# Performance work log

Measured on AMD Instinct MI355X. Metric: run time of the kernel, lower is better.

## Reference

```python
import jax, jax.numpy as jnp
import numpy as np

N_HEAD = 16
N_EMBD = 1024
B, T = 4, 1024


def setup_inputs() -> dict:
    key = jax.random.key(0)
    ks = jax.random.split(key, 8)
    hs = N_EMBD // N_HEAD
    x = jax.random.normal(ks[0], (B, T, N_EMBD), dtype=jnp.float32)
    # previous-layer attention load per token, ~O(1/T) like a softmax column mean
    refractory_state = jax.random.uniform(ks[1], (B, T), dtype=jnp.float32) / T
    s_attn = 1.0 / np.sqrt(N_EMBD)
    W_attn = jax.random.normal(ks[2], (N_EMBD, 3 * N_EMBD), dtype=jnp.float32) * s_attn
    b_attn = jnp.zeros((3 * N_EMBD,), dtype=jnp.float32)
    W_proj = jax.random.normal(ks[3], (N_EMBD, N_EMBD), dtype=jnp.float32) * s_attn
    b_proj = jnp.zeros((N_EMBD,), dtype=jnp.float32)
    # learnable LIF params, init per module (lif_mode='refractory')
    threshold = jnp.full((N_HEAD,), 0.01, dtype=jnp.float32)
    leak = jnp.full((N_HEAD,), 2.0, dtype=jnp.float32)
    steepness = jnp.full((N_HEAD,), 2.0, dtype=jnp.float32)
    ref_strength = jnp.full((N_HEAD,), -2.0, dtype=jnp.float32)
    cross_w = jnp.full((N_HEAD,), -2.0, dtype=jnp.float32)
    return {
        "x": x, "refractory_state": refractory_state,
        "W_attn": W_attn, "b_attn": b_attn,
        "W_proj": W_proj, "b_proj": b_proj,
        "threshold": threshold, "leak": leak, "steepness": steepness,
        "ref_strength": ref_strength, "cross_w": cross_w,
    }


def reference(x, refractory_state, W_attn, b_attn, W_proj, b_proj,
              threshold, leak, steepness, ref_strength, cross_w):
    Bq, Tq, C = x.shape
    H = N_HEAD
    hs = C // H
    qkv = x @ W_attn + b_attn                     # [B,T,3C]
    q, k, v = jnp.split(qkv, 3, axis=-1)
    q = q.reshape(Bq, Tq, H, hs).transpose(0, 2, 1, 3)  # [B,H,T,hs]
    k = k.reshape(Bq, Tq, H, hs).transpose(0, 2, 1, 3)
    v = v.reshape(Bq, Tq, H, hs).transpose(0, 2, 1, 3)

    att = jnp.einsum('bhqd,bhkd->bhqk', q, k) * (1.0 / jnp.sqrt(jnp.asarray(hs, x.dtype)))
    causal = jnp.tril(jnp.ones((Tq, Tq), dtype=bool))
    att = jnp.where(causal[None, None], att, -jnp.inf)
    probs = jax.nn.softmax(att, axis=-1)          # [B,H,T,T]

    thr = (jnp.abs(threshold) * 0.1)[None, :, None, None]
    lk = jax.nn.sigmoid(leak)[None, :, None, None]
    st = jax.nn.softplus(steepness)[None, :, None, None]
    # refractory: column load over queries + cross-layer load
    column_load = probs.mean(axis=-2, keepdims=True)          # [B,H,1,T]
    eff_thr = thr + jax.nn.softplus(ref_strength)[None, :, None, None] * column_load
    eff_thr = eff_thr + jax.nn.sigmoid(cross_w)[None, :, None, None] * refractory_state[:, None, None, :]

    fire = jax.nn.sigmoid(st * (probs - eff_thr))
    lif_w = fire + lk * (1.0 - fire)
    mod = probs * lif_w
    mod = mod / (mod.sum(axis=-1, keepdims=True) + 1e-8)
    new_refractory = mod.mean(axis=1).mean(axis=-2)           # [B,T]

    y = jnp.einsum('bhqk,bhkd->bhqd', mod, v)
    y = y.transpose(0, 2, 1, 3).reshape(Bq, Tq, C)
    y = y @ W_proj + b_proj
    return y, new_refractory
```

## Files before the change

kernel.cpp:

```cpp
#include <hip/hip_runtime.h>
#include <math.h>

#define B_  4
#define T_  1024
#define C_  1024
#define H_  16
#define HS_ 64
#define K2E 0.1803368801f
#define LOG2E 1.44269504f

typedef _Float16 f16;
typedef _Float16 f16x8 __attribute__((ext_vector_type(8)));
typedef _Float16 f16x4 __attribute__((ext_vector_type(4)));
typedef float f32x4 __attribute__((ext_vector_type(4)));

#define MFMA16(a,b,c) __builtin_amdgcn_mfma_f32_16x16x32_f16(a,b,c,0,0,0)
#define EXP2(x) __builtin_amdgcn_exp2f(x)
#define RCP(x)  __builtin_amdgcn_rcpf(x)

#define PSTRIDE_BH 557056

__device__ __forceinline__ float qsum_(float v){
    v += __shfl_xor(v,1,64); v += __shfl_xor(v,2,64);
    v += __shfl_xor(v,4,64); v += __shfl_xor(v,8,64);
    return v;
}
__device__ __forceinline__ float sigmoidf_(float x){ return 1.0f/(1.0f + __expf(-x)); }
__device__ __forceinline__ float softplusf_(float x){ return fmaxf(x, 0.0f) + log1pf(__expf(-fabsf(x))); }

__device__ __forceinline__ void gload_lds16(const f16* g, f16* l){
    __builtin_amdgcn_global_load_lds(
        (__attribute__((address_space(1))) void*)(void*)g,
        (__attribute__((address_space(3))) void*)(void*)l, 16, 0, 0);
}

__global__ __launch_bounds__(256) void prep_k(
    const float* __restrict__ x, const float* __restrict__ Wa,
    const float* __restrict__ Wp,
    f16* __restrict__ x_h, f16* __restrict__ WaT, f16* __restrict__ WpT,
    float* __restrict__ zbase)
{
    __shared__ float tl[32][33];
    const int bid = blockIdx.x, tid = threadIdx.x;
    if (bid < 2048){
        int i = bid*256 + tid;
        const float4* p = (const float4*)x + (size_t)i*2;
        float4 a = p[0], b = p[1];
        f16x8 o;
        o[0]=(f16)a.x; o[1]=(f16)a.y; o[2]=(f16)a.z; o[3]=(f16)a.w;
        o[4]=(f16)b.x; o[5]=(f16)b.y; o[6]=(f16)b.z; o[7]=(f16)b.w;
        *((f16x8*)x_h + i) = o;
    } else if (bid < 5120){
        int t = bid - 2048;
        int n0 = (t % 96)*32, k0 = (t / 96)*32;
        const int c = tid & 31, r4 = tid >> 5;
        #pragma unroll
        for (int i=0;i<4;i++){ int r = r4*4+i; tl[r][c] = Wa[(size_t)(k0+r)*3072 + n0 + c]; }
        __syncthreads();
        #pragma unroll
        for (int i=0;i<4;i++){ int r = r4*4+i; WaT[(size_t)(n0+r)*1024 + k0 + c] = (f16)tl[c][r]; }
    } else if (bid < 6144){
        int t = bid - 5120;
        int n0 = (t & 31)*32, k0 = (t >> 5)*32;
        const int c = tid & 31, r4 = tid >> 5;
        #pragma unroll
        for (int i=0;i<4;i++){ int r = r4*4+i; tl[r][c] = Wp[(size_t)(k0+r)*1024 + n0 + c]; }
        __syncthreads();
        #pragma unroll
        for (int i=0;i<4;i++){ int r = r4*4+i; WpT[(size_t)(n0+r)*1024 + k0 + c] = (f16)tl[c][r]; }
    } else {
        int idx = (bid - 6144)*256 + tid;
        float4 z; z.x=0.f; z.y=0.f; z.z=0.f; z.w=0.f;
        ((float4*)zbase)[idx] = z;
    }
}

#define CT_STRIDE 132
__global__ __launch_bounds__(256) void gemm_qkv_k(
    const f16* __restrict__ A, const f16* __restrict__ Bt,
    const float* __restrict__ bias,
    f16* __restrict__ Qh, f16* __restrict__ Kh, f16* __restrict__ Vt)
{
    __shared__ __align__(16) f16 smem[16896];
    const int tid = threadIdx.x;
    const int lane = tid & 63, wave = tid >> 6;
    const int lx = lane & 15, quad = lane >> 4;
    const int wm = wave & 1, wn = wave >> 1;
    const int lin = blockIdx.y*24 + blockIdx.x;
    const int nb  = (lin & 7)*96 + (lin >> 3);
    const int m0 = (nb/24)*128, n0 = (nb%24)*128;
    const f16* Ap = A  + (size_t)m0*1024;
    const f16* Bp = Bt + (size_t)n0*1024;
    f32x4 acc[4][4];
    #pragma unroll
    for (int i=0;i<4;i++){
        #pragma unroll
        for (int j=0;j<4;j++){ acc[i][j][0]=0.f;acc[i][j][1]=0.f;acc[i][j][2]=0.f;acc[i][j][3]=0.f; }
    }
#define GQ_STAGE(BUF, KT) { \
    const int k0s = (KT)*32; \
    for (int i=0;i<2;i++){ int c=i*4+wave; \
        gload_lds16(Ap + (size_t)(c*16+lx)*1024 + k0s + quad*8, &smem[(BUF) + c*512]); \
        gload_lds16(Bp + (size_t)(c*16+lx)*1024 + k0s + quad*8, &smem[(BUF) + 4096 + c*512]); } }
#define GQ_COMP(BUF) { \
    f16x8 af[4], bf[4]; \
    for (int mt=0;mt<4;mt++) af[mt] = *(const f16x8*)&smem[(BUF) + (wm*4+mt)*512 + quad*128 + lx*8]; \
    for (int nt=0;nt<4;nt++) bf[nt] = *(const f16x8*)&smem[(BUF) + 4096 + (wn*4+nt)*512 + quad*128 + lx*8]; \
    for (int mt=0;mt<4;mt++) \
        for (int nt=0;nt<4;nt++) \
            acc[mt][nt] = MFMA16(af[mt], bf[nt], acc[mt][nt]); }

    GQ_STAGE(0, 0);
    __syncthreads();
    #pragma unroll 1
    for (int it=0; it<32; it+=2){
        if (it+1 < 32) GQ_STAGE(8192, it+1);
        GQ_COMP(0);
        __syncthreads();
        if (it+2 < 32) GQ_STAGE(0, it+2);
        GQ_COMP(8192);
        __syncthreads();
    }
    f16* Ct = smem;
    #pragma unroll
    for (int mt=0;mt<4;mt++){
        #pragma unroll
        for (int nt=0;nt<4;nt++){
            int n_loc = wn*64 + nt*16 + lx;
            float bv = bias[n0 + n_loc];
            #pragma unroll
            for (int r=0;r<4;r++){
                int m_loc = wm*64 + mt*16 + quad*4 + r;
                Ct[m_loc*CT_STRIDE + n_loc] = (f16)(acc[mt][nt][r] + bv);
            }
        }
    }
    __syncthreads();
    const int bb = m0 >> 10;
    if (n0 < 2048){
        for (int it=0; it<8; it++){
            int row = it*32 + wave*8 + (lane>>3);
            int ch  = lane & 7;
            int m_loc = row >> 1, half = row & 1;
            f16x8 v = *(const f16x8*)&Ct[m_loc*CT_STRIDE + half*64 + ch*8];
            int n = n0 + half*64;
            int which = n >> 10, cc = n & 1023, h = cc >> 6;
            int t = (m0 + m_loc) & 1023;
            f16* dst = (which==0) ? Qh : Kh;
            *(f16x8*)(dst + ((size_t)(bb*16+h)*1024 + t)*64 + ch*8) = v;
        }
    } else {
        for (int it=0; it<8; it++){
            int drow = it*16 + wave*4 + (lane>>4);
            int ch   = lane & 15;
            int cc = (n0 + drow) & 1023;
            int h = cc >> 6, d = cc & 63;
            f16 tmp[8];
            #pragma unroll
            for (int j=0;j<8;j++) tmp[j] = Ct[(ch*8+j)*CT_STRIDE + drow];
            int t = (m0 + ch*8) & 1023;
            *(f16x8*)(Vt + ((size_t)(bb*16+h)*64 + d)*1024 + t) = *(f16x8*)tmp;
        }
    }
}

__global__ __launch_bounds__(256) void gemm_proj_k(
    const f16* __restrict__ A, const f16* __restrict__ Bt,
    const float* __restrict__ bias, float* __restrict__ out,
    const float* __restrict__ racc)
{
    if (blockIdx.x == 512){
        float* oref = out + (size_t)B_*T_*C_;
        #pragma unroll
        for (int j=0;j<16;j++){
            int idx = j*256 + threadIdx.x;
            oref[idx] = racc[idx] * (1.0f/(H_*T_));
        }
        return;
    }
    __shared__ __align__(16) f16 smem[12288];
    const int tid = threadIdx.x;
    const int lane = tid & 63, wave = tid >> 6;
    const int lx = lane & 15, quad = lane >> 4;
    const int wm = wave & 1, wn = wave >> 1;
    const int m0 = (blockIdx.x >> 4)*128, n0 = (blockIdx.x & 15)*64;
    const f16* Ap = A  + (size_t)m0*1024;
    const f16* Bp = Bt + (size_t)n0*1024;
    f32x4 acc[4][2];
    #pragma unroll
    for (int i=0;i<4;i++){
        #pragma unroll
        for (int j=0;j<2;j++){ acc[i][j][0]=0.f;acc[i][j][1]=0.f;acc[i][j][2]=0.f;acc[i][j][3]=0.f; }
    }
#define GP_LOAD(rA,rB,K0) { \
    for (int i=0;i<2;i++) \
        rA[i] = *(const f16x8*)(Ap + (size_t)((i*4+wave)*16+lx)*1024 + (K0) + quad*8); \
    rB = *(const f16x8*)(Bp + (size_t)(wave*16+lx)*1024 + (K0) + quad*8); }
#define GP_STORE(rA,rB,BUF) { \
    for (int i=0;i<2;i++) \
        *(f16x8*)&smem[(BUF) + (i*4+wave)*512 + quad*128 + lx*8] = rA[i]; \
    *(f16x8*)&smem[(BUF) + 4096 + wave*512 + quad*128 + lx*8] = rB; }
#define GP_COMP(BUF) { \
    f16x8 af[4], bf[2]; \
    for (int mt=0;mt<4;mt++) af[mt] = *(const f16x8*)&smem[(BUF) + (wm*4+mt)*512 + quad*128 + lx*8]; \
    for (int nt=0;nt<2;nt++) bf[nt] = *(const f16x8*)&smem[(BUF) + 4096 + (wn*2+nt)*512 + quad*128 + lx*8]; \
    for (int mt=0;mt<4;mt++) \
        for (int nt=0;nt<2;nt++) \
            acc[mt][nt] = MFMA16(af[mt], bf[nt], acc[mt][nt]); }

    f16x8 raE[2], raO[2], rbE, rbO;
    GP_LOAD(raE, rbE, 0);
    GP_STORE(raE, rbE, 0);
    GP_LOAD(raO, rbO, 32);
    __syncthreads();
    #pragma unroll 1
    for (int it=0; it<32; it+=2){
        if (it+2 < 32) GP_LOAD(raE, rbE, (it+2)*32);
        GP_STORE(raO, rbO, 6144);
        GP_COMP(0);
        __syncthreads();
        if (it+3 < 32) GP_LOAD(raO, rbO, (it+3)*32);
        if (it+2 < 32) GP_STORE(raE, rbE, 0);
        GP_COMP(6144);
        __syncthreads();
    }
    #pragma unroll
    for (int mt=0;mt<4;mt++){
        #pragma unroll
        for (int nt=0;nt<2;nt++){
            int n = n0 + wn*32 + nt*16 + lx;
            float bv = bias[n];
            #pragma unroll
            for (int r=0;r<4;r++){
                int m = m0 + wm*64 + mt*16 + quad*4 + r;
                out[(size_t)m*1024 + n] = acc[mt][nt][r] + bv;
            }
        }
    }
}

__global__ __launch_bounds__(256) void attn_stats_k(
    const f16* __restrict__ Qh, const f16* __restrict__ Kh,
    float* __restrict__ rowl, float* __restrict__ colp,
    f16* __restrict__ Pbuf)
{
    __shared__ __align__(16) f16 Kl[8192];
    __shared__ __align__(16) f16 Pl[4][16*72];
    __shared__ float invl_sh[64];
    const int tid = threadIdx.x;
    const int lane = tid & 63, wave = tid >> 6;
    const int lx = lane & 15, quad = lane >> 4;
    const int g  = 15 - (blockIdx.x >> 6);
    const int bh = blockIdx.x & 63;
    const int qpos = wave*16 + quad*4;
    const size_t kbase = (size_t)bh*65536;
    const int S = (g+1)*64;
    f16* __restrict__ Pblk = Pbuf + (size_t)bh*PSTRIDE_BH + (size_t)4096*((g*(g+1))>>1);

    const size_t qoff = ((size_t)bh*1024 + g*64 + wave*16 + lx)*64;
    f16x8 aq0 = *(const f16x8*)(Qh + qoff + quad*8);
    f16x8 aq1 = *(const f16x8*)(Qh + qoff + 32 + quad*8);

#define KLOAD(dst, KT) { \
    for (int i=0;i<2;i++){ int u=i*4+wave, cc=u&3, kh=u>>2; \
        dst[i] = *(const f16x8*)(Kh + kbase + (size_t)((KT)*64 + cc*16+lx)*64 + kh*32 + quad*8); } }
#define KSTORE(src, BUF) { \
    for (int i=0;i<2;i++){ int u=i*4+wave, cc=u&3, kh=u>>2; \
        *(f16x8*)&Kl[(BUF) + cc*1024 + kh*512 + quad*128 + lx*8] = src[i]; } }
#define STATS1_TILE(KT, BUF) { \
    const bool diag = ((KT) == g); \
    for (int nt=0;nt<4;nt++){ \
        f32x4 sc = {0.f,0.f,0.f,0.f}; \
        f16x8 b0 = *(const f16x8*)&Kl[(BUF) + nt*1024 + quad*128 + lx*8]; \
        f16x8 b1 = *(const f16x8*)&Kl[(BUF) + nt*1024 + 512 + quad*128 + lx*8]; \
        sc = MFMA16(aq0, b0, sc); \
        sc = MFMA16(aq1, b1, sc); \
        for (int r=0;r<4;r++){ \
            float sv = sc[r]; \
            if (diag && (nt*16+lx) > (qpos + r)) sv = -1e4f; \
            float p = EXP2(sv*K2E); \
            ls[r] += p; \
            Pl[wave][(quad*4+r)*72 + nt*16 + lx] = (f16)p; \
        } } \
    for (int it2=0; it2<2; it2++){ \
        int qq = it2*8 + (lane>>3), chh = lane & 7; \
        f16x8 v = *(const f16x8*)&Pl[wave][qq*72 + chh*8]; \
        *(f16x8*)(Pblk + (size_t)(wave*16+qq)*S + (KT)*64 + chh*8) = v; } }

    f16x8 rkE[2], rkO[2];
    float ls[4] = {0.f,0.f,0.f,0.f};
    KLOAD(rkE, 0);
    KSTORE(rkE, 0);
    if (g >= 1) KLOAD(rkO, 1);
    __syncthreads();
    #pragma unroll 1
    for (int kt=0; kt<=g; kt+=2){
        if (kt+2 <= g) KLOAD(rkE, kt+2);
        if (kt+1 <= g) KSTORE(rkO, 4096);
        STATS1_TILE(kt, 0);
        __syncthreads();
        if (kt+1 <= g){
            if (kt+3 <= g) KLOAD(rkO, kt+3);
            if (kt+2 <= g) KSTORE(rkE, 0);
            STATS1_TILE(kt+1, 4096);
            __syncthreads();
        }
    }
    #pragma unroll
    for (int r=0;r<4;r++){
        float l = qsum_(ls[r]);
        if (lx == 0){
            rowl[(size_t)bh*1024 + g*64 + qpos + r] = l;
            invl_sh[qpos + r] = RCP(l);
        }
    }
    __syncthreads();
    if (tid < (g+1)*16){
        const int k0 = tid*4;
        float a0=0.f, a1=0.f, a2=0.f, a3=0.f;
        const f16* pr = Pblk + k0;
        #pragma unroll 4
        for (int q=0;q<64;q++){
            f16x4 v = *(const f16x4*)(pr + (size_t)q*S);
            float w = invl_sh[q];
            a0 += (float)v[0]*w; a1 += (float)v[1]*w;
            a2 += (float)v[2]*w; a3 += (float)v[3]*w;
        }
        float* cp = colp + (size_t)bh*1024 + k0;
        atomicAdd(cp+0,a0); atomicAdd(cp+1,a1);
        atomicAdd(cp+2,a2); atomicAdd(cp+3,a3);
    }
}

__global__ __launch_bounds__(256) void attn_apply_k(
    const f16* __restrict__ Vt,
    const float* __restrict__ rowl,
    const float* __restrict__ colp, const float* __restrict__ refr,
    const float* __restrict__ threshold, const float* __restrict__ leak,
    const float* __restrict__ steepness, const float* __restrict__ ref_strength,
    const float* __restrict__ cross_w,
    f16* __restrict__ Yh, float* __restrict__ racc,
    f16* __restrict__ Pbuf)
{
    __shared__ __align__(16) f16 Vl[8192];
    __shared__ __align__(16) f16 Pl[4][16*72];
    __shared__ float eb[1024];
    __shared__ float invl_sh[64];
    __shared__ float invD_sh[64];
    const int tid = threadIdx.x;
    const int lane = tid & 63, wave = tid >> 6;
    const int lx = lane & 15, quad = lane >> 4;
    const int qr8 = lane >> 3, c8 = lane & 7;
    const int g  = 15 - (blockIdx.x >> 6);
    const int bh = blockIdx.x & 63;
    const int b  = bh >> 4, h = bh & 15;
    const size_t kbase = (size_t)bh*65536;
    const int S = (g+1)*64;
    f16* __restrict__ Pblk = Pbuf + (size_t)bh*PSTRIDE_BH + (size_t)4096*((g*(g+1))>>1);

    const float thr = fabsf(threshold[h])*0.1f;
    const float lk  = sigmoidf_(leak[h]);
    const float st2 = softplusf_(steepness[h]) * LOG2E;
    const float sprT= softplusf_(ref_strength[h]) * (1.0f/T_);
    const float cw  = sigmoidf_(cross_w[h]);
    const float Alk = 1.f - lk;

    {
        float4 cp = *(const float4*)(colp + (size_t)bh*1024 + tid*4);
        float4 rf = *(const float4*)(refr + (size_t)b*1024 + tid*4);
        eb[tid*4+0] = st2*(thr + sprT*cp.x + cw*rf.x);
        eb[tid*4+1] = st2*(thr + sprT*cp.y + cw*rf.y);
        eb[tid*4+2] = st2*(thr + sprT*cp.z + cw*rf.z);
        eb[tid*4+3] = st2*(thr + sprT*cp.w + cw*rf.w);
    }
    if (tid < 64) invl_sh[tid] = RCP(rowl[(size_t)bh*1024 + g*64 + tid]);
    __syncthreads();

    const float w0 = invl_sh[wave*16 + qr8];
    const float w1 = invl_sh[wave*16 + 8 + qr8];

    f32x4 y[4];
    #pragma unroll
    for (int i=0;i<4;i++){ y[i][0]=0.f;y[i][1]=0.f;y[i][2]=0.f;y[i][3]=0.f; }
    float Dp0 = 0.f, Dp1 = 0.f;

#define VLOAD(dst, KT) { \
    for (int i=0;i<2;i++){ int u=i*4+wave, cc=u&3, kh=u>>2; \
        dst[i] = *(const f16x8*)(Vt + kbase + (size_t)(cc*16+lx)*1024 + (KT)*64 + kh*32 + quad*8); } }
#define VSTORE(src, BUF) { \
    for (int i=0;i<2;i++){ int u=i*4+wave, cc=u&3, kh=u>>2; \
        *(f16x8*)&Vl[(BUF) + cc*1024 + kh*512 + quad*128 + lx*8] = src[i]; } }
#define PLOAD(dst, KT) { \
    dst[0] = *(const f16x8*)(Pblk + (size_t)(wave*16 + qr8)*S + (KT)*64 + c8*8); \
    dst[1] = *(const f16x8*)(Pblk + (size_t)(wave*16 + 8 + qr8)*S + (KT)*64 + c8*8); }
#define APPLY1_TILE(KT, BUF, pv) { \
    float ebv[8]; \
    *(float4*)&ebv[0] = *(const float4*)&eb[(KT)*64 + c8*8]; \
    *(float4*)&ebv[4] = *(const float4*)&eb[(KT)*64 + c8*8 + 4]; \
    f16x8 o0, o1; \
    for (int j=0;j<8;j++){ \
        float pj = (float)pv[0][j] * w0; \
        float fire = RCP(1.f + EXP2(ebv[j] - st2*pj)); \
        float pw = pj*(lk + Alk*fire); \
        Dp0 += pw; o0[j] = (f16)pw; } \
    for (int j=0;j<8;j++){ \
        float pj = (float)pv[1][j] * w1; \
        float fire = RCP(1.f + EXP2(ebv[j] - st2*pj)); \
        float pw = pj*(lk + Alk*fire); \
        Dp1 += pw; o1[j] = (f16)pw; } \
    *(f16x8*)&Pl[wave][qr8*72 + c8*8] = o0; \
    *(f16x8*)&Pl[wave][(8+qr8)*72 + c8*8] = o1; \
    { f16x8 ap0 = *(const f16x8*)&Pl[wave][lx*72 + quad*8]; \
      f16x8 ap1 = *(const f16x8*)&Pl[wave][lx*72 + 32 + quad*8]; \
      for (int dt=0;dt<4;dt++){ \
        f16x8 bv0 = *(const f16x8*)&Vl[(BUF) + dt*1024 + quad*128 + lx*8]; \
        f16x8 bv1 = *(const f16x8*)&Vl[(BUF) + dt*1024 + 512 + quad*128 + lx*8]; \
        y[dt] = MFMA16(ap0, bv0, y[dt]); \
        y[dt] = MFMA16(ap1, bv1, y[dt]); } } }

    f16x8 rvE[2], rvO[2], pvE[2], pvO[2];
    VLOAD(rvE, 0); PLOAD(pvE, 0);
    VSTORE(rvE, 0);
    if (g >= 1){ VLOAD(rvO, 1); PLOAD(pvO, 1); }
    __syncthreads();
    #pragma unroll 1
    for (int kt=0; kt<=g; kt+=2){
        if (kt+2 <= g) VLOAD(rvE, kt+2);
        if (kt+1 <= g) VSTORE(rvO, 4096);
        APPLY1_TILE(kt, 0, pvE);
        if (kt+2 <= g) PLOAD(pvE, kt+2);
        __syncthreads();
        if (kt+1 <= g){
            if (kt+3 <= g) VLOAD(rvO, kt+3);
            if (kt+2 <= g) VSTORE(rvE, 0);
            APPLY1_TILE(kt+1, 4096, pvO);
            if (kt+3 <= g) PLOAD(pvO, kt+3);
            __syncthreads();
        }
    }
    Dp0 += __shfl_xor(Dp0,1,64); Dp0 += __shfl_xor(Dp0,2,64); Dp0 += __shfl_xor(Dp0,4,64);
    Dp1 += __shfl_xor(Dp1,1,64); Dp1 += __shfl_xor(Dp1,2,64); Dp1 += __shfl_xor(Dp1,4,64);
    if (c8 == 0){
        invD_sh[wave*16 + qr8]     = RCP(Dp0 + 1e-8f);
        invD_sh[wave*16 + 8 + qr8] = RCP(Dp1 + 1e-8f);
    }
    __syncthreads();

    float invD[4];
    #pragma unroll
    for (int r=0;r<4;r++) invD[r] = invD_sh[wave*16 + quad*4 + r];
    #pragma unroll
    for (int dt=0;dt<4;dt++){
        #pragma unroll
        for (int r=0;r<4;r++)
            Pl[wave][(quad*4+r)*72 + dt*16 + lx] = (f16)(y[dt][r]*invD[r]);
    }
    #pragma unroll
    for (int it=0; it<2; it++){
        int q = it*8 + (lane>>3), ch = lane & 7;
        f16x8 v = *(const f16x8*)&Pl[wave][q*72 + ch*8];
        *(f16x8*)(Yh + (size_t)(b*1024 + g*64 + wave*16 + q)*1024 + h*64 + ch*8) = v;
    }

    if (tid < (g+1)*16){
        const int k0 = tid*4;
        float4 ebv = *(const float4*)&eb[k0];
        float a0=0.f, a1=0.f, a2=0.f, a3=0.f;
        const f16* pr = Pblk + k0;
        #pragma unroll 4
        for (int q=0;q<64;q++){
            f16x4 v = *(const f16x4*)(pr + (size_t)q*S);
            float wl = invl_sh[q], wd = invD_sh[q];
            float p0 = (float)v[0]*wl, p1 = (float)v[1]*wl;
            float p2 = (float)v[2]*wl, p3 = (float)v[3]*wl;
            float f0 = RCP(1.f + EXP2(ebv.x - st2*p0));
            float f1 = RCP(1.f + EXP2(ebv.y - st2*p1));
            float f2 = RCP(1.f + EXP2(ebv.z - st2*p2));
            float f3 = RCP(1.f + EXP2(ebv.w - st2*p3));
            a0 += p0*(lk + Alk*f0)*wd; a1 += p1*(lk + Alk*f1)*wd;
            a2 += p2*(lk + Alk*f2)*wd; a3 += p3*(lk + Alk*f3)*wd;
        }
        float* rp = racc + (size_t)b*1024 + k0;
        atomicAdd(rp+0,a0); atomicAdd(rp+1,a1);
        atomicAdd(rp+2,a2); atomicAdd(rp+3,a3);
    }
}

extern "C" void kernel_launch(void* const* d_in, const int* in_sizes, int n_in,
                              void* d_out, int out_size, void* d_ws, size_t ws_size,
                              hipStream_t stream) {
    (void)in_sizes; (void)n_in; (void)out_size; (void)ws_size;
    const float* x           = (const float*)d_in[0];
    const float* refr        = (const float*)d_in[1];
    const float* W_attn      = (const float*)d_in[2];
    const float* b_attn      = (const float*)d_in[3];
    const float* W_proj      = (const float*)d_in[4];
    const float* b_proj      = (const float*)d_in[5];
    const float* threshold   = (const float*)d_in[6];
    const float* leak        = (const float*)d_in[7];
    const float* steepness   = (const float*)d_in[8];
    const float* ref_strength= (const float*)d_in[9];
    const float* cross_w     = (const float*)d_in[10];
    float* out = (float*)d_out;

    char* ws = (char*)d_ws;
    f16* x_h = (f16*)ws;                       ws += (size_t)4096*1024*2;
    f16* WaT = (f16*)ws;                       ws += (size_t)3072*1024*2;
    f16* WpT = (f16*)ws;                       ws += (size_t)1024*1024*2;
    f16* Qh  = (f16*)ws;                       ws += (size_t)64*1024*64*2;
    f16* Kh  = (f16*)ws;                       ws += (size_t)64*1024*64*2;
    f16* Vt  = (f16*)ws;                       ws += (size_t)64*64*1024*2;
    f16* Yh  = (f16*)ws;                       ws += (size_t)4096*1024*2;
    float* rowl = (float*)ws;                  ws += (size_t)65536*4;
    float* colp = (float*)ws;                  ws += (size_t)65536*4;
    float* racc = (float*)ws;                  ws += (size_t)4096*4;
    f16* Pbuf = (f16*)ws;                      ws += (size_t)64*PSTRIDE_BH*2;

    prep_k<<<dim3(6212), dim3(256), 0, stream>>>(x, W_attn, W_proj, x_h, WaT, WpT, colp);
    gemm_qkv_k<<<dim3(24,32), dim3(256), 0, stream>>>(x_h, WaT, b_attn, Qh, Kh, Vt);
    attn_stats_k<<<dim3(1024), dim3(256), 0, stream>>>(Qh, Kh, rowl, colp, Pbuf);
    attn_apply_k<<<dim3(1024), dim3(256), 0, stream>>>(
        Vt, rowl, colp, refr,
        threshold, leak, steepness, ref_strength, cross_w, Yh, racc, Pbuf);
    gemm_proj_k<<<dim3(513), dim3(256), 0, stream>>>(Yh, WpT, b_proj, out, racc);
}
```

Measured before the change: 261.6 us.

## Pair causal row blocks per workgroup, remap proj GEMM tiles, use direct LDS loads

The attention stats and apply kernels now process two query blocks per workgroup (g = 15-j and g = j), so every block does the same amount of causal work and the grid is halved to 512. The projection GEMM swizzles its block index to change tile ordering across CUs. It also stages A/B tiles with a direct global-to-LDS load helper instead of a register round trip. The intent is to remove tail imbalance from triangular work and to cut register and VGPR staging cost, at the price of fewer blocks and less prefetch distance in the GEMM.

```diff
diff --git a/kernel.cpp b/kernel.cpp
--- a/kernel.cpp
+++ b/kernel.cpp
@@ -183,7 +183,9 @@
     const int lane = tid & 63, wave = tid >> 6;
     const int lx = lane & 15, quad = lane >> 4;
     const int wm = wave & 1, wn = wave >> 1;
-    const int m0 = (blockIdx.x >> 4)*128, n0 = (blockIdx.x & 15)*64;
+    const int lin = blockIdx.x;
+    const int nb  = (lin & 7)*64 + (lin >> 3);
+    const int m0 = (nb >> 4)*128, n0 = (nb & 15)*64;
     const f16* Ap = A  + (size_t)m0*1024;
     const f16* Bp = Bt + (size_t)n0*1024;
     f32x4 acc[4][2];
@@ -192,14 +194,11 @@
         #pragma unroll
         for (int j=0;j<2;j++){ acc[i][j][0]=0.f;acc[i][j][1]=0.f;acc[i][j][2]=0.f;acc[i][j][3]=0.f; }
     }
-#define GP_LOAD(rA,rB,K0) { \
-    for (int i=0;i<2;i++) \
-        rA[i] = *(const f16x8*)(Ap + (size_t)((i*4+wave)*16+lx)*1024 + (K0) + quad*8); \
-    rB = *(const f16x8*)(Bp + (size_t)(wave*16+lx)*1024 + (K0) + quad*8); }
-#define GP_STORE(rA,rB,BUF) { \
-    for (int i=0;i<2;i++) \
-        *(f16x8*)&smem[(BUF) + (i*4+wave)*512 + quad*128 + lx*8] = rA[i]; \
-    *(f16x8*)&smem[(BUF) + 4096 + wave*512 + quad*128 + lx*8] = rB; }
+#define GP_STAGE(BUF, KT) { \
+    const int k0s = (KT)*32; \
+    for (int i=0;i<2;i++){ int c=i*4+wave; \
+        gload_lds16(Ap + (size_t)(c*16+lx)*1024 + k0s + quad*8, &smem[(BUF) + c*512]); } \
+    gload_lds16(Bp + (size_t)(wave*16+lx)*1024 + k0s + quad*8, &smem[(BUF) + 4096 + wave*512]); }
 #define GP_COMP(BUF) { \
     f16x8 af[4], bf[2]; \
     for (int mt=0;mt<4;mt++) af[mt] = *(const f16x8*)&smem[(BUF) + (wm*4+mt)*512 + quad*128 + lx*8]; \
@@ -208,19 +207,14 @@
         for (int nt=0;nt<2;nt++) \
             acc[mt][nt] = MFMA16(af[mt], bf[nt], acc[mt][nt]); }
 
-    f16x8 raE[2], raO[2], rbE, rbO;
-    GP_LOAD(raE, rbE, 0);
-    GP_STORE(raE, rbE, 0);
-    GP_LOAD(raO, rbO, 32);
+    GP_STAGE(0, 0);
     __syncthreads();
     #pragma unroll 1
     for (int it=0; it<32; it+=2){
-        if (it+2 < 32) GP_LOAD(raE, rbE, (it+2)*32);
-        GP_STORE(raO, rbO, 6144);
+        if (it+1 < 32) GP_STAGE(6144, it+1);
         GP_COMP(0);
         __syncthreads();
-        if (it+3 < 32) GP_LOAD(raO, rbO, (it+3)*32);
-        if (it+2 < 32) GP_STORE(raE, rbE, 0);
+        if (it+2 < 32) GP_STAGE(0, it+2);
         GP_COMP(6144);
         __syncthreads();
     }
@@ -250,16 +244,10 @@
     const int tid = threadIdx.x;
     const int lane = tid & 63, wave = tid >> 6;
     const int lx = lane & 15, quad = lane >> 4;
-    const int g  = 15 - (blockIdx.x >> 6);
+    const int j  = blockIdx.x >> 6;
     const int bh = blockIdx.x & 63;
     const int qpos = wave*16 + quad*4;
     const size_t kbase = (size_t)bh*65536;
-    const int S = (g+1)*64;
-    f16* __restrict__ Pblk = Pbuf + (size_t)bh*PSTRIDE_BH + (size_t)4096*((g*(g+1))>>1);
-
-    const size_t qoff = ((size_t)bh*1024 + g*64 + wave*16 + lx)*64;
-    f16x8 aq0 = *(const f16x8*)(Qh + qoff + quad*8);
-    f16x8 aq1 = *(const f16x8*)(Qh + qoff + 32 + quad*8);
 
 #define KLOAD(dst, KT) { \
     for (int i=0;i<2;i++){ int u=i*4+wave, cc=u&3, kh=u>>2; \
@@ -287,48 +275,58 @@
         f16x8 v = *(const f16x8*)&Pl[wave][qq*72 + chh*8]; \
         *(f16x8*)(Pblk + (size_t)(wave*16+qq)*S + (KT)*64 + chh*8) = v; } }
 
-    f16x8 rkE[2], rkO[2];
-    float ls[4] = {0.f,0.f,0.f,0.f};
-    KLOAD(rkE, 0);
-    KSTORE(rkE, 0);
-    if (g >= 1) KLOAD(rkO, 1);
-    __syncthreads();
     #pragma unroll 1
-    for (int kt=0; kt<=g; kt+=2){
-        if (kt+2 <= g) KLOAD(rkE, kt+2);
-        if (kt+1 <= g) KSTORE(rkO, 4096);
-        STATS1_TILE(kt, 0);
-        __syncthreads();
-        if (kt+1 <= g){
-            if (kt+3 <= g) KLOAD(rkO, kt+3);
-            if (kt+2 <= g) KSTORE(rkE, 0);
-            STATS1_TILE(kt+1, 4096);
+    for (int pass=0; pass<2; ++pass){
+        const int g = pass ? j : (15 - j);
+        const int S = (g+1)*64;
+        f16* __restrict__ Pblk = Pbuf + (size_t)bh*PSTRIDE_BH + (size_t)4096*((g*(g+1))>>1);
+        const size_t qoff = ((size_t)bh*1024 + g*64 + wave*16 + lx)*64;
+        f16x8 aq0 = *(const f16x8*)(Qh + qoff + quad*8);
+        f16x8 aq1 = *(const f16x8*)(Qh + qoff + 32 + quad*8);
+
+        f16x8 rkE[2], rkO[2];
+        float ls[4] = {0.f,0.f,0.f,0.f};
+        KLOAD(rkE, 0);
+        KSTORE(rkE, 0);
+        if (g >= 1) KLOAD(rkO, 1);
+        __syncthreads();
+        #pragma unroll 1
+        for (int kt=0; kt<=g; kt+=2){
+            if (kt+2 <= g) KLOAD(rkE, kt+2);
+            if (kt+1 <= g) KSTORE(rkO, 4096);
+            STATS1_TILE(kt, 0);
             __syncthreads();
-        }
-    }
-    #pragma unroll
-    for (int r=0;r<4;r++){
-        float l = qsum_(ls[r]);
-        if (lx == 0){
-            rowl[(size_t)bh*1024 + g*64 + qpos + r] = l;
-            invl_sh[qpos + r] = RCP(l);
-        }
-    }
-    __syncthreads();
-    if (tid < (g+1)*16){
-        const int k0 = tid*4;
-        float a0=0.f, a1=0.f, a2=0.f, a3=0.f;
-        const f16* pr = Pblk + k0;
-        #pragma unroll 4
-        for (int q=0;q<64;q++){
-            f16x4 v = *(const f16x4*)(pr + (size_t)q*S);
-            float w = invl_sh[q];
-            a0 += (float)v[0]*w; a1 += (float)v[1]*w;
-            a2 += (float)v[2]*w; a3 += (float)v[3]*w;
-        }
-        float* cp = colp + (size_t)bh*1024 + k0;
-        atomicAdd(cp+0,a0); atomicAdd(cp+1,a1);
-        atomicAdd(cp+2,a2); atomicAdd(cp+3,a3);
+            if (kt+1 <= g){
+                if (kt+3 <= g) KLOAD(rkO, kt+3);
+                if (kt+2 <= g) KSTORE(rkE, 0);
+                STATS1_TILE(kt+1, 4096);
+                __syncthreads();
+            }
+        }
+        #pragma unroll
+        for (int r=0;r<4;r++){
+            float l = qsum_(ls[r]);
+            if (lx == 0){
+                rowl[(size_t)bh*1024 + g*64 + qpos + r] = l;
+                invl_sh[qpos + r] = RCP(l);
+            }
+        }
+        __syncthreads();
+        if (tid < (g+1)*16){
+            const int k0 = tid*4;
+            float a0=0.f, a1=0.f, a2=0.f, a3=0.f;
+            const f16* pr = Pblk + k0;
+            #pragma unroll 4
+            for (int q=0;q<64;q++){
+                f16x4 v = *(const f16x4*)(pr + (size_t)q*S);
+                float w = invl_sh[q];
+                a0 += (float)v[0]*w; a1 += (float)v[1]*w;
+                a2 += (float)v[2]*w; a3 += (float)v[3]*w;
+            }
+            float* cp = colp + (size_t)bh*1024 + k0;
+            atomicAdd(cp+0,a0); atomicAdd(cp+1,a1);
+            atomicAdd(cp+2,a2); atomicAdd(cp+3,a3);
+        }
     }
 }
 
@@ -351,12 +349,10 @@
     const int lane = tid & 63, wave = tid >> 6;
     const int lx = lane & 15, quad = lane >> 4;
     const int qr8 = lane >> 3, c8 = lane & 7;
-    const int g  = 15 - (blockIdx.x >> 6);
+    const int j  = blockIdx.x >> 6;
     const int bh = blockIdx.x & 63;
     const int b  = bh >> 4, h = bh & 15;
     const size_t kbase = (size_t)bh*65536;
-    const int S = (g+1)*64;
-    f16* __restrict__ Pblk = Pbuf + (size_t)bh*PSTRIDE_BH + (size_t)4096*((g*(g+1))>>1);
 
     const float thr = fabsf(threshold[h])*0.1f;
     const float lk  = sigmoidf_(leak[h]);
@@ -373,16 +369,6 @@
         eb[tid*4+2] = st2*(thr + sprT*cp.z + cw*rf.z);
         eb[tid*4+3] = st2*(thr + sprT*cp.w + cw*rf.w);
     }
-    if (tid < 64) invl_sh[tid] = RCP(rowl[(size_t)bh*1024 + g*64 + tid]);
-    __syncthreads();
-
-    const float w0 = invl_sh[wave*16 + qr8];
-    const float w1 = invl_sh[wave*16 + 8 + qr8];
-
-    f32x4 y[4];
-    #pragma unroll
-    for (int i=0;i<4;i++){ y[i][0]=0.f;y[i][1]=0.f;y[i][2]=0.f;y[i][3]=0.f; }
-    float Dp0 = 0.f, Dp1 = 0.f;
 
 #define VLOAD(dst, KT) { \
     for (int i=0;i<2;i++){ int u=i*4+wave, cc=u&3, kh=u>>2; \
@@ -398,16 +384,16 @@
     *(float4*)&ebv[0] = *(const float4*)&eb[(KT)*64 + c8*8]; \
     *(float4*)&ebv[4] = *(const float4*)&eb[(KT)*64 + c8*8 + 4]; \
     f16x8 o0, o1; \
-    for (int j=0;j<8;j++){ \
-        float pj = (float)pv[0][j] * w0; \
-        float fire = RCP(1.f + EXP2(ebv[j] - st2*pj)); \
+    for (int jj=0;jj<8;jj++){ \
+        float pj = (float)pv[0][jj] * w0; \
+        float fire = RCP(1.f + EXP2(ebv[jj] - st2*pj)); \
         float pw = pj*(lk + Alk*fire); \
-        Dp0 += pw; o0[j] = (f16)pw; } \
-    for (int j=0;j<8;j++){ \
-        float pj = (float)pv[1][j] * w1; \
-        float fire = RCP(1.f + EXP2(ebv[j] - st2*pj)); \
+        Dp0 += pw; o0[jj] = (f16)pw; } \
+    for (int jj=0;jj<8;jj++){ \
+        float pj = (float)pv[1][jj] * w1; \
+        float fire = RCP(1.f + EXP2(ebv[jj] - st2*pj)); \
         float pw = pj*(lk + Alk*fire); \
-        Dp1 += pw; o1[j] = (f16)pw; } \
+        Dp1 += pw; o1[jj] = (f16)pw; } \
     *(f16x8*)&Pl[wave][qr8*72 + c8*8] = o0; \
     *(f16x8*)&Pl[wave][(8+qr8)*72 + c8*8] = o1; \
     { f16x8 ap0 = *(const f16x8*)&Pl[wave][lx*72 + quad*8]; \
@@ -418,71 +404,90 @@
         y[dt] = MFMA16(ap0, bv0, y[dt]); \
         y[dt] = MFMA16(ap1, bv1, y[dt]); } } }
 
-    f16x8 rvE[2], rvO[2], pvE[2], pvO[2];
-    VLOAD(rvE, 0); PLOAD(pvE, 0);
-    VSTORE(rvE, 0);
-    if (g >= 1){ VLOAD(rvO, 1); PLOAD(pvO, 1); }
-    __syncthreads();
     #pragma unroll 1
-    for (int kt=0; kt<=g; kt+=2){
-        if (kt+2 <= g) VLOAD(rvE, kt+2);
-        if (kt+1 <= g) VSTORE(rvO, 4096);
-        APPLY1_TILE(kt, 0, pvE);
-        if (kt+2 <= g) PLOAD(pvE, kt+2);
-        __syncthreads();
-        if (kt+1 <= g){
-            if (kt+3 <= g) VLOAD(rvO, kt+3);
-            if (kt+2 <= g) VSTORE(rvE, 0);
-            APPLY1_TILE(kt+1, 4096, pvO);
-            if (kt+3 <= g) PLOAD(pvO, kt+3);
+    for (int pass=0; pass<2; ++pass){
+        const int g = pass ? j : (15 - j);
+        const int S = (g+1)*64;
+        f16* __restrict__ Pblk = Pbuf + (size_t)bh*PSTRIDE_BH + (size_t)4096*((g*(g+1))>>1);
+
+        __syncthreads();
+        if (tid < 64) invl_sh[tid] = RCP(rowl[(size_t)bh*1024 + g*64 + tid]);
+        __syncthreads();
+
+        const float w0 = invl_sh[wave*16 + qr8];
+        const float w1 = invl_sh[wave*16 + 8 + qr8];
+
+        f32x4 y[4];
+        #pragma unroll
+        for (int i=0;i<4;i++){ y[i][0]=0.f;y[i][1]=0.f;y[i][2]=0.f;y[i][3]=0.f; }
+        float Dp0 = 0.f, Dp1 = 0.f;
+
+        f16x8 rvE[2], rvO[2], pvE[2], pvO[2];
+        VLOAD(rvE, 0); PLOAD(pvE, 0);
+        VSTORE(rvE, 0);
+        if (g >= 1){ VLOAD(rvO, 1); PLOAD(pvO, 1); }
+        __syncthreads();
+        #pragma unroll 1
+        for (int kt=0; kt<=g; kt+=2){
+            if (kt+2 <= g) VLOAD(rvE, kt+2);
+            if (kt+1 <= g) VSTORE(rvO, 4096);
+            APPLY1_TILE(kt, 0, pvE);
+            if (kt+2 <= g) PLOAD(pvE, kt+2);
             __syncthreads();
-        }
-    }
-    Dp0 += __shfl_xor(Dp0,1,64); Dp0 += __shfl_xor(Dp0,2,64); Dp0 += __shfl_xor(Dp0,4,64);
-    Dp1 += __shfl_xor(Dp1,1,64); Dp1 += __shfl_xor(Dp1,2,64); Dp1 += __shfl_xor(Dp1,4,64);
-    if (c8 == 0){
-        invD_sh[wave*16 + qr8]     = RCP(Dp0 + 1e-8f);
-        invD_sh[wave*16 + 8 + qr8] = RCP(Dp1 + 1e-8f);
-    }
-    __syncthreads();
-
-    float invD[4];
-    #pragma unroll
-    for (int r=0;r<4;r++) invD[r] = invD_sh[wave*16 + quad*4 + r];
-    #pragma unroll
-    for (int dt=0;dt<4;dt++){
-        #pragma unroll
-        for (int r=0;r<4;r++)
-            Pl[wave][(quad*4+r)*72 + dt*16 + lx] = (f16)(y[dt][r]*invD[r]);
-    }
-    #pragma unroll
-    for (int it=0; it<2; it++){
-        int q = it*8 + (lane>>3), ch = lane & 7;
-        f16x8 v = *(const f16x8*)&Pl[wave][q*72 + ch*8];
-        *(f16x8*)(Yh + (size_t)(b*1024 + g*64 + wave*16 + q)*1024 + h*64 + ch*8) = v;
-    }
-
-    if (tid < (g+1)*16){
-        const int k0 = tid*4;
-        float4 ebv = *(const float4*)&eb[k0];
-        float a0=0.f, a1=0.f, a2=0.f, a3=0.f;
-        const f16* pr = Pblk + k0;
-        #pragma unroll 4
-        for (int q=0;q<64;q++){
-            f16x4 v = *(const f16x4*)(pr + (size_t)q*S);
-            float wl = invl_sh[q], wd = invD_sh[q];
-            float p0 = (float)v[0]*wl, p1 = (float)v[1]*wl;
-            float p2 = (float)v[2]*wl, p3 = (float)v[3]*wl;
-            float f0 = RCP(1.f + EXP2(ebv.x - st2*p0));
-            float f1 = RCP(1.f + EXP2(ebv.y - st2*p1));
-            float f2 = RCP(1.f + EXP2(ebv.z - st2*p2));
-            float f3 = RCP(1.f + EXP2(ebv.w - st2*p3));
-            a0 += p0*(lk + Alk*f0)*wd; a1 += p1*(lk + Alk*f1)*wd;
-            a2 += p2*(lk + Alk*f2)*wd; a3 += p3*(lk + Alk*f3)*wd;
-        }
-        float* rp = racc + (size_t)b*1024 + k0;
-        atomicAdd(rp+0,a0); atomicAdd(rp+1,a1);
-        atomicAdd(rp+2,a2); atomicAdd(rp+3,a3);
+            if (kt+1 <= g){
+                if (kt+3 <= g) VLOAD(rvO, kt+3);
+                if (kt+2 <= g) VSTORE(rvE, 0);
+                APPLY1_TILE(kt+1, 4096, pvO);
+                if (kt+3 <= g) PLOAD(pvO, kt+3);
+                __syncthreads();
+            }
+        }
+        Dp0 += __shfl_xor(Dp0,1,64); Dp0 += __shfl_xor(Dp0,2,64); Dp0 += __shfl_xor(Dp0,4,64);
+        Dp1 += __shfl_xor(Dp1,1,64); Dp1 += __shfl_xor(Dp1,2,64); Dp1 += __shfl_xor(Dp1,4,64);
+        if (c8 == 0){
+            invD_sh[wave*16 + qr8]     = RCP(Dp0 + 1e-8f);
+            invD_sh[wave*16 + 8 + qr8] = RCP(Dp1 + 1e-8f);
+        }
+        __syncthreads();
+
+        float invD[4];
+        #pragma unroll
+        for (int r=0;r<4;r++) invD[r] = invD_sh[wave*16 + quad*4 + r];
+        #pragma unroll
+        for (int dt=0;dt<4;dt++){
+            #pragma unroll
+            for (int r=0;r<4;r++)
+                Pl[wave][(quad*4+r)*72 + dt*16 + lx] = (f16)(y[dt][r]*invD[r]);
+        }
+        #pragma unroll
+        for (int it=0; it<2; it++){
+            int q = it*8 + (lane>>3), ch = lane & 7;
+            f16x8 v = *(const f16x8*)&Pl[wave][q*72 + ch*8];
+            *(f16x8*)(Yh + (size_t)(b*1024 + g*64 + wave*16 + q)*1024 + h*64 + ch*8) = v;
+        }
+
+        if (tid < (g+1)*16){
+            const int k0 = tid*4;
+            float4 ebv = *(const float4*)&eb[k0];
+            float a0=0.f, a1=0.f, a2=0.f, a3=0.f;
+            const f16* pr = Pblk + k0;
+            #pragma unroll 4
+            for (int q=0;q<64;q++){
+                f16x4 v = *(const f16x4*)(pr + (size_t)q*S);
+                float wl = invl_sh[q], wd = invD_sh[q];
+                float p0 = (float)v[0]*wl, p1 = (float)v[1]*wl;
+                float p2 = (float)v[2]*wl, p3 = (float)v[3]*wl;
+                float f0 = RCP(1.f + EXP2(ebv.x - st2*p0));
+                float f1 = RCP(1.f + EXP2(ebv.y - st2*p1));
+                float f2 = RCP(1.f + EXP2(ebv.z - st2*p2));
+                float f3 = RCP(1.f + EXP2(ebv.w - st2*p3));
+                a0 += p0*(lk + Alk*f0)*wd; a1 += p1*(lk + Alk*f1)*wd;
+                a2 += p2*(lk + Alk*f2)*wd; a3 += p3*(lk + Alk*f3)*wd;
+            }
+            float* rp = racc + (size_t)b*1024 + k0;
+            atomicAdd(rp+0,a0); atomicAdd(rp+1,a1);
+            atomicAdd(rp+2,a2); atomicAdd(rp+3,a3);
+        }
     }
 }
 
@@ -518,8 +523,8 @@
 
     prep_k<<<dim3(6212), dim3(256), 0, stream>>>(x, W_attn, W_proj, x_h, WaT, WpT, colp);
     gemm_qkv_k<<<dim3(24,32), dim3(256), 0, stream>>>(x_h, WaT, b_attn, Qh, Kh, Vt);
-    attn_stats_k<<<dim3(1024), dim3(256), 0, stream>>>(Qh, Kh, rowl, colp, Pbuf);
-    attn_apply_k<<<dim3(1024), dim3(256), 0, stream>>>(
+    attn_stats_k<<<dim3(512), dim3(256), 0, stream>>>(Qh, Kh, rowl, colp, Pbuf);
+    attn_apply_k<<<dim3(512), dim3(256), 0, stream>>>(
         Vt, rowl, colp, refr,
         threshold, leak, steepness, ref_strength, cross_w, Yh, racc, Pbuf);
     gemm_proj_k<<<dim3(513), dim3(256), 0, stream>>>(Yh, WpT, b_proj, out, racc);
```

Measured after the change: 268.8 us. 1.03x slower.
